# Kernel optimization log

Hardware: AMD Instinct MI355X
Metric: run time of the kernel (lower is better)

## Reference

```python
import jax, jax.numpy as jnp
import numpy as np

B, S, D, H = 4, 2048, 1024, 16
HD = D // H


def setup_inputs() -> dict:
    key = jax.random.key(0)
    ks = jax.random.split(key, 12)
    sc = 0.02
    inp = {
        "q": jax.random.normal(ks[0], (B, S, D), jnp.float32),
        "k": jax.random.normal(ks[1], (B, S, D), jnp.float32),
        "v": jax.random.normal(ks[2], (B, S, D), jnp.float32),
        "mask": jnp.tril(jnp.ones((S, S), jnp.int32))[None, None],  # causal [1,1,S,S]
        "Wq": jax.random.normal(ks[3], (D, D), jnp.float32) * sc,
        "bq": jnp.zeros((D,), jnp.float32),
        "Wk": jax.random.normal(ks[4], (D, D), jnp.float32) * sc,
        "bk": jnp.zeros((D,), jnp.float32),
        "Wv": jax.random.normal(ks[5], (D, D), jnp.float32) * sc,
        "bv": jnp.zeros((D,), jnp.float32),
        "Wo": jax.random.normal(ks[6], (D, D), jnp.float32) * sc,
        "bo": jnp.zeros((D,), jnp.float32),
    }
    return inp


def reference(q, k, v, mask, Wq, bq, Wk, bk, Wv, bv, Wo, bo):
    # Linear projections (torch Linear: x @ W.T + b)
    qh = (q @ Wq.T + bq).reshape(B, S, H, HD).transpose(0, 2, 1, 3)  # [B,H,S,hd]
    kh = (k @ Wk.T + bk).reshape(B, S, H, HD).transpose(0, 2, 1, 3)
    vh = (v @ Wv.T + bv).reshape(B, S, H, HD).transpose(0, 2, 1, 3)
    score = jnp.einsum("bhqd,bhkd->bhqk", qh, kh) / jnp.sqrt(jnp.float32(HD))
    score = jnp.where(mask == 0, jnp.float32(-10000.0), score)
    attn = jax.nn.softmax(score, axis=-1)
    out = jnp.einsum("bhqk,bhkd->bhqd", attn, vh)  # [B,H,S,hd]
    out = out.transpose(0, 2, 1, 3).reshape(B, S, D)
    return out @ Wo.T + bo
```

## Files before the change

### kernel.cpp

```cpp
#include <hip/hip_runtime.h>

#define S_LEN 2048
#define D_DIM 1024
#define NB    4
#define NH    16
#define HDIM  64
#define QSCL  0.18033688011112042f

typedef float  f32x4  __attribute__((ext_vector_type(4)));
typedef __bf16 bf16x4 __attribute__((ext_vector_type(4)));
typedef __bf16 bf16x8 __attribute__((ext_vector_type(8)));
typedef unsigned int u32x2 __attribute__((ext_vector_type(2)));
typedef unsigned int u32x4 __attribute__((ext_vector_type(4)));

static __device__ __forceinline__ f32x4 mfma16(bf16x8 a, bf16x8 b, f32x4 c) {
  return __builtin_amdgcn_mfma_f32_16x16x32_bf16(a, b, c, 0, 0, 0);
}
static __device__ __forceinline__ bf16x4 cvt4(f32x4 v) {
  return __builtin_convertvector(v, bf16x4);
}
static __device__ __forceinline__ bf16x8 cvt8(f32x4 lo, f32x4 hi) {
  bf16x4 a = cvt4(lo), b = cvt4(hi);
  bf16x8 r;
  r[0] = a[0]; r[1] = a[1]; r[2] = a[2]; r[3] = a[3];
  r[4] = b[0]; r[5] = b[1]; r[6] = b[2]; r[7] = b[3];
  return r;
}
static __device__ __forceinline__ void cp16(const void* g, void* l) {
  __builtin_amdgcn_global_load_lds(
      (const __attribute__((address_space(1))) unsigned int*)g,
      (__attribute__((address_space(3))) unsigned int*)l, 16, 0, 0);
}

__global__ __launch_bounds__(256) void conv_w(
    const float* __restrict__ Wq, const float* __restrict__ Wk,
    const float* __restrict__ Wv, const float* __restrict__ Wo,
    __bf16* __restrict__ out)
{
  const float* src;
  if (blockIdx.y == 0) src = Wq;
  else if (blockIdx.y == 1) src = Wk;
  else if (blockIdx.y == 2) src = Wv;
  else src = Wo;
  size_t i = ((size_t)blockIdx.x * 256 + threadIdx.x) * 4;
  f32x4 v = *(const f32x4*)(src + i);
  *(bf16x4*)(out + (size_t)blockIdx.y * (D_DIM * D_DIM) + i) = cvt4(v);
}

__global__ __launch_bounds__(256) void conv_a(
    const float* __restrict__ q, const float* __restrict__ k,
    const float* __restrict__ v, __bf16* __restrict__ out)
{
  const float* src;
  if (blockIdx.y == 0) src = q;
  else if (blockIdx.y == 1) src = k;
  else src = v;
  size_t i = ((size_t)blockIdx.x * 256 + threadIdx.x) * 4;
  f32x4 x = *(const f32x4*)(src + i);
  *(bf16x4*)(out + (size_t)blockIdx.y * ((size_t)NB * S_LEN * D_DIM) + i) = cvt4(x);
}

static __device__ __forceinline__ void proj_epilogue(
    f32x4 (&acc)[4][4], int z, int mbase, int nbase, int wm, int wn,
    int l15, int quad, const float* bias,
    __bf16* qh, __bf16* kh, __bf16* vt)
{
  const float scl = (z == 0) ? QSCL : 1.0f;
#pragma unroll
  for (int mt = 0; mt < 4; ++mt)
#pragma unroll
    for (int nt = 0; nt < 4; ++nt) {
      int n = nbase + wn + nt * 16 + l15;
      int h = n >> 6, hd = n & 63;
      float bb = bias[n];
      f32x4 vv = acc[mt][nt];
#pragma unroll
      for (int r = 0; r < 4; ++r) vv[r] = (vv[r] + bb) * scl;
      bf16x4 pv = cvt4(vv);
      int m0 = mbase + wm + mt * 16 + quad * 4;
      int b = m0 >> 11, s0 = m0 & 2047;
      if (z == 2) {
        *(bf16x4*)(vt + ((size_t)((b * NH + h) * HDIM + hd)) * S_LEN + s0) = pv;
      } else {
        __bf16* out = (z == 0) ? qh : kh;
#pragma unroll
        for (int r = 0; r < 4; ++r)
          out[((size_t)(b * NH + h) * S_LEN + s0 + r) * HDIM + hd] = pv[r];
      }
    }
}

__global__ __launch_bounds__(256, 4) void proj_bf16(
    const __bf16* __restrict__ abf, const __bf16* __restrict__ Wbf,
    const float* __restrict__ bq, const float* __restrict__ bk, const float* __restrict__ bv,
    __bf16* __restrict__ qh, __bf16* __restrict__ kh, __bf16* __restrict__ vt)
{
  const __bf16* A = abf + (size_t)blockIdx.z * ((size_t)NB * S_LEN * D_DIM);
  const __bf16* W = Wbf + (size_t)blockIdx.z * (D_DIM * D_DIM);
  const float* bias = (blockIdx.z == 0) ? bq : (blockIdx.z == 1) ? bk : bv;

  __shared__ __bf16 As[128 * 64];
  __shared__ __bf16 Bs[128 * 64];

  const int tid  = threadIdx.x;
  const int wave = tid >> 6;
  const int lane = tid & 63;
  const int l15  = lane & 15;
  const int quad = lane >> 4;
  const int mbase = blockIdx.x * 128;
  const int nbase = blockIdx.y * 128;
  const int wm = (wave & 1) * 64;
  const int wn = (wave >> 1) * 64;
  const int brow = lane >> 3;
  const int scol = ((lane & 7) ^ (brow & 7)) * 8;
  const int swz  = l15 & 7;

  f32x4 acc[4][4] = {};

  for (int kt = 0; kt < D_DIM; kt += 64) {
#pragma unroll
    for (int c = 0; c < 4; ++c) {
      int r = wave * 32 + c * 8 + brow;
      cp16(A + (size_t)(mbase + r) * D_DIM + kt + scol, As + r * 64);
      cp16(W + (size_t)(nbase + r) * D_DIM + kt + scol, Bs + r * 64);
    }
    __syncthreads();

#pragma unroll
    for (int k0 = 0; k0 < 2; ++k0) {
      bf16x8 af[4], bfr[4];
#pragma unroll
      for (int i = 0; i < 4; ++i) {
        int off = ((k0 * 4 + quad) ^ swz) * 8;
        af[i]  = *(const bf16x8*)(As + (wm + i * 16 + l15) * 64 + off);
        bfr[i] = *(const bf16x8*)(Bs + (wn + i * 16 + l15) * 64 + off);
      }
#pragma unroll
      for (int mt = 0; mt < 4; ++mt)
#pragma unroll
        for (int nt = 0; nt < 4; ++nt)
          acc[mt][nt] = mfma16(af[mt], bfr[nt], acc[mt][nt]);
    }
    __syncthreads();
  }

  proj_epilogue(acc, blockIdx.z, mbase, nbase, wm, wn, l15, quad, bias, qh, kh, vt);
}

__global__ __launch_bounds__(256, 2) void proj_f32(
    const float* __restrict__ qin, const float* __restrict__ kin, const float* __restrict__ vin,
    const __bf16* __restrict__ Wbf,
    const float* __restrict__ bq, const float* __restrict__ bk, const float* __restrict__ bv,
    __bf16* __restrict__ qh, __bf16* __restrict__ kh, __bf16* __restrict__ vt)
{
  const float* A; const float* bias;
  if (blockIdx.z == 0)      { A = qin; bias = bq; }
  else if (blockIdx.z == 1) { A = kin; bias = bk; }
  else                      { A = vin; bias = bv; }
  const __bf16* W = Wbf + (size_t)blockIdx.z * (D_DIM * D_DIM);

  __shared__ float  As[128 * 64];
  __shared__ __bf16 Bs[128 * 64];

  const int tid  = threadIdx.x;
  const int wave = tid >> 6;
  const int lane = tid & 63;
  const int l15  = lane & 15;
  const int quad = lane >> 4;
  const int mbase = blockIdx.x * 128;
  const int nbase = blockIdx.y * 128;
  const int wm = (wave & 1) * 64;
  const int wn = (wave >> 1) * 64;
  const int arow = lane >> 4;
  const int brow = lane >> 3;

  f32x4 acc[4][4] = {};

  for (int kt = 0; kt < D_DIM; kt += 64) {
#pragma unroll
    for (int c = 0; c < 8; ++c) {
      int rr = c * 4 + arow;
      int r  = wave * 32 + rr;
      int col = ((lane & 15) ^ (rr & 15)) * 4;
      cp16(A + (size_t)(mbase + r) * D_DIM + kt + col, As + r * 64);
    }
#pragma unroll
    for (int c = 0; c < 4; ++c) {
      int r  = wave * 32 + c * 8 + brow;
      int col = ((lane & 7) ^ (brow & 7)) * 8;
      cp16(W + (size_t)(nbase + r) * D_DIM + kt + col, Bs + r * 64);
    }
    __syncthreads();

#pragma unroll
    for (int k0 = 0; k0 < 2; ++k0) {
      bf16x8 af[4], bfr[4];
#pragma unroll
      for (int i = 0; i < 4; ++i) {
        const float* ap = As + (wm + i * 16 + l15) * 64;
        int c0 = k0 * 8 + quad * 2;
        f32x4 lo = *(const f32x4*)(ap + ((c0 ^ l15) * 4));
        f32x4 hi = *(const f32x4*)(ap + (((c0 + 1) ^ l15) * 4));
        af[i] = cvt8(lo, hi);
        bfr[i] = *(const bf16x8*)(Bs + (wn + i * 16 + l15) * 64 +
                                  (((k0 * 4 + quad) ^ (l15 & 7)) * 8));
      }
#pragma unroll
      for (int mt = 0; mt < 4; ++mt)
#pragma unroll
        for (int nt = 0; nt < 4; ++nt)
          acc[mt][nt] = mfma16(af[mt], bfr[nt], acc[mt][nt]);
    }
    __syncthreads();
  }

  proj_epilogue(acc, blockIdx.z, mbase, nbase, wm, wn, l15, quad, bias, qh, kh, vt);
}

__global__ __launch_bounds__(256, 4) void attn_kernel(
    const __bf16* __restrict__ qh, const __bf16* __restrict__ kh,
    const __bf16* __restrict__ vt, __bf16* __restrict__ ao)
{
  __shared__ __bf16 Kb[2][64 * 64];
  __shared__ __bf16 Vb[2][64 * 64];

  const int lin = blockIdx.x + (blockIdx.y << 4);
  const int xcd = lin & 7;
  const int idx = lin >> 3;
  const int u   = idx & 15;
  const int x   = (u & 1) ? (15 - (u >> 1)) : (u >> 1);
  const int bh  = xcd * 8 + (idx >> 4);

  const int qc0 = x, qc1 = 31 - x;
  const int last = qc1;

  const __bf16* qp = qh + (size_t)bh * S_LEN * HDIM;
  const __bf16* kp = kh + (size_t)bh * S_LEN * HDIM;
  const __bf16* vp = vt + (size_t)bh * HDIM * S_LEN;

  const int tid  = threadIdx.x;
  const int wave = tid >> 6;
  const int lane = tid & 63;
  const int l15  = lane & 15;
  const int quad = lane >> 4;
  const int w16  = wave * 16;
  const int srow = lane >> 3;
  const int scol = ((lane & 7) ^ srow) * 8;
  const int swz  = l15 & 7;
  const int b = bh >> 4, h = bh & 15;

  const int srcA = l15 + ((lane & 16) << 1);
  const int srcB = srcA + 16;
  const bool hiq = (lane & 32) != 0;

  bf16x8 fq[2][2];
#pragma unroll
  for (int j = 0; j < 2; ++j) {
    const int qb = (j ? qc1 : qc0) * 64;
    const __bf16* qrow = qp + (size_t)(qb + w16 + l15) * HDIM;
    fq[j][0] = *(const bf16x8*)(qrow + quad * 8);
    fq[j][1] = *(const bf16x8*)(qrow + 32 + quad * 8);
  }

  f32x4 accO[2][4] = {};
  float lp[2] = {0.f, 0.f};

#pragma unroll
  for (int c = 0; c < 2; ++c) {
    int rb = w16 + c * 8;
    cp16(kp + (size_t)(rb + srow) * HDIM + scol,  &Kb[0][rb * 64]);
    cp16(vp + (size_t)(rb + srow) * S_LEN + scol, &Vb[0][rb * 64]);
  }

  int cur = 0;
  for (int kt = 0; kt <= last; ++kt) {
    __syncthreads();

    if (kt < last) {
#pragma unroll
      for (int c = 0; c < 2; ++c) {
        int rb = w16 + c * 8;
        cp16(kp + (size_t)((kt + 1) * 64 + rb + srow) * HDIM + scol,
             &Kb[cur ^ 1][rb * 64]);
        cp16(vp + (size_t)(rb + srow) * S_LEN + (kt + 1) * 64 + scol,
             &Vb[cur ^ 1][rb * 64]);
      }
    }

    const __bf16* Kc = &Kb[cur][0];
    const __bf16* Vc = &Vb[cur][0];
    const bool act0 = (kt <= qc0);

    f32x4 sc[2][4] = {};
#pragma unroll
    for (int k0 = 0; k0 < 2; ++k0)
#pragma unroll
      for (int nt = 0; nt < 4; ++nt) {
        bf16x8 bk = *(const bf16x8*)(Kc + (nt * 16 + l15) * 64 +
                                     (((k0 * 4 + quad) ^ swz) * 8));
        if (act0) sc[0][nt] = mfma16(bk, fq[0][k0], sc[0][nt]);
        sc[1][nt] = mfma16(bk, fq[1][k0], sc[1][nt]);
      }

    bf16x8 pa[2][2];
#pragma unroll
    for (int j = 0; j < 2; ++j) {
      if (j == 0 && !act0) continue;
      const int qcj = j ? qc1 : qc0;
      unsigned int d0[4], d1[4];
      float lsn[4];
#pragma unroll
      for (int nt = 0; nt < 4; ++nt) {
        f32x4 p;
#pragma unroll
        for (int r = 0; r < 4; ++r) p[r] = __builtin_amdgcn_exp2f(sc[j][nt][r]);
        if (kt == qcj) {
#pragma unroll
          for (int r = 0; r < 4; ++r)
            if (nt * 16 + quad * 4 + r > w16 + l15) p[r] = 0.f;
        }
        lsn[nt] = (p[0] + p[1]) + (p[2] + p[3]);
        u32x2 w = __builtin_bit_cast(u32x2, cvt4(p));
        d0[nt] = w[0]; d1[nt] = w[1];
      }
      lp[j] += (lsn[0] + lsn[1]) + (lsn[2] + lsn[3]);

      u32x4 A0, A1;
#pragma unroll
      for (int dw = 0; dw < 4; ++dw) {
        const unsigned int* dd = (dw & 1) ? d1 : d0;
        const int src = (dw < 2) ? srcA : srcB;
        unsigned int t0 = (unsigned int)__shfl((int)dd[0], src);
        unsigned int t1 = (unsigned int)__shfl((int)dd[1], src);
        unsigned int t2 = (unsigned int)__shfl((int)dd[2], src);
        unsigned int t3 = (unsigned int)__shfl((int)dd[3], src);
        A0[dw] = hiq ? t1 : t0;
        A1[dw] = hiq ? t3 : t2;
      }
      pa[j][0] = __builtin_bit_cast(bf16x8, A0);
      pa[j][1] = __builtin_bit_cast(bf16x8, A1);
    }

#pragma unroll
    for (int k0 = 0; k0 < 2; ++k0)
#pragma unroll
      for (int nt = 0; nt < 4; ++nt) {
        bf16x8 bv = *(const bf16x8*)(Vc + (nt * 16 + l15) * 64 +
                                     (((k0 * 4 + quad) ^ swz) * 8));
        if (act0) accO[0][nt] = mfma16(pa[0][k0], bv, accO[0][nt]);
        accO[1][nt] = mfma16(pa[1][k0], bv, accO[1][nt]);
      }

    cur ^= 1;
  }

#pragma unroll
  for (int j = 0; j < 2; ++j) {
    float lf = lp[j];
    lf += __shfl_xor(lf, 16);
    lf += __shfl_xor(lf, 32);
    const int qb = (j ? qc1 : qc0) * 64;
#pragma unroll
    for (int r = 0; r < 4; ++r) {
      float inv = 1.0f / __shfl(lf, quad * 4 + r);
#pragma unroll
      for (int nt = 0; nt < 4; ++nt) accO[j][nt][r] *= inv;
    }
#pragma unroll
    for (int nt = 0; nt < 4; ++nt) {
      bf16x4 ob = cvt4(accO[j][nt]);
#pragma unroll
      for (int r = 0; r < 4; ++r) {
        int sr = qb + w16 + quad * 4 + r;
        ao[((size_t)b * S_LEN + sr) * D_DIM + h * HDIM + nt * 16 + l15] = ob[r];
      }
    }
  }
}

__global__ __launch_bounds__(256, 4) void out_gemm(
    const __bf16* __restrict__ Ain, const __bf16* __restrict__ Wbf,
    const float* __restrict__ bo, float* __restrict__ Cout)
{
  __shared__ __bf16 As[128 * 64];
  __shared__ __bf16 Bs[128 * 64];

  const int tid  = threadIdx.x;
  const int wave = tid >> 6;
  const int lane = tid & 63;
  const int l15  = lane & 15;
  const int quad = lane >> 4;
  const int mbase = blockIdx.x * 128;
  const int nbase = blockIdx.y * 128;
  const int wm = (wave & 1) * 64;
  const int wn = (wave >> 1) * 64;
  const int brow = lane >> 3;
  const int scol = ((lane & 7) ^ (brow & 7)) * 8;
  const int swz  = l15 & 7;

  f32x4 acc[4][4] = {};

  for (int kt = 0; kt < D_DIM; kt += 64) {
#pragma unroll
    for (int c = 0; c < 4; ++c) {
      int r = wave * 32 + c * 8 + brow;
      cp16(Ain + (size_t)(mbase + r) * D_DIM + kt + scol, As + r * 64);
      cp16(Wbf + (size_t)(nbase + r) * D_DIM + kt + scol, Bs + r * 64);
    }
    __syncthreads();

#pragma unroll
    for (int k0 = 0; k0 < 2; ++k0) {
      bf16x8 af[4], bfr[4];
#pragma unroll
      for (int i = 0; i < 4; ++i) {
        int off = ((k0 * 4 + quad) ^ swz) * 8;
        af[i]  = *(const bf16x8*)(As + (wm + i * 16 + l15) * 64 + off);
        bfr[i] = *(const bf16x8*)(Bs + (wn + i * 16 + l15) * 64 + off);
      }
#pragma unroll
      for (int mt = 0; mt < 4; ++mt)
#pragma unroll
        for (int nt = 0; nt < 4; ++nt)
          acc[mt][nt] = mfma16(af[mt], bfr[nt], acc[mt][nt]);
    }
    __syncthreads();
  }

#pragma unroll
  for (int mt = 0; mt < 4; ++mt)
#pragma unroll
    for (int nt = 0; nt < 4; ++nt) {
      int n = nbase + wn + nt * 16 + l15;
      float bb = bo[n];
      int m0 = mbase + wm + mt * 16 + quad * 4;
#pragma unroll
      for (int r = 0; r < 4; ++r)
        Cout[(size_t)(m0 + r) * D_DIM + n] = acc[mt][nt][r] + bb;
    }
}

extern "C" void kernel_launch(void* const* d_in, const int* in_sizes, int n_in,
                              void* d_out, int out_size, void* d_ws, size_t ws_size,
                              hipStream_t stream) {
  const float* q  = (const float*)d_in[0];
  const float* k  = (const float*)d_in[1];
  const float* v  = (const float*)d_in[2];
  const float* Wq = (const float*)d_in[4];
  const float* bq = (const float*)d_in[5];
  const float* Wk = (const float*)d_in[6];
  const float* bk = (const float*)d_in[7];
  const float* Wv = (const float*)d_in[8];
  const float* bv = (const float*)d_in[9];
  const float* Wo = (const float*)d_in[10];
  const float* bo = (const float*)d_in[11];

  __bf16* ws = (__bf16*)d_ws;
  const size_t WSZ = (size_t)D_DIM * D_DIM;
  const size_t NE  = (size_t)NB * S_LEN * D_DIM;
  __bf16* wbf = ws;
  __bf16* qh  = ws + 4 * WSZ;
  __bf16* kh  = qh + NE;
  __bf16* vt  = kh + NE;
  __bf16* ao  = vt + NE;
  __bf16* abf = vt + NE;
  const size_t NEED = (size_t)(4 * WSZ + 6 * NE) * sizeof(__bf16);

  const bool useBf16A = (ws_size >= NEED);

  conv_w<<<dim3(1024, 4), 256, 0, stream>>>(Wq, Wk, Wv, Wo, wbf);
  if (useBf16A) {
    conv_a<<<dim3(8192, 3), 256, 0, stream>>>(q, k, v, abf);
    proj_bf16<<<dim3(64, 8, 3), 256, 0, stream>>>(abf, wbf, bq, bk, bv, qh, kh, vt);
  } else {
    proj_f32<<<dim3(64, 8, 3), 256, 0, stream>>>(q, k, v, wbf, bq, bk, bv, qh, kh, vt);
  }
  attn_kernel<<<dim3(16, 64), 256, 0, stream>>>(qh, kh, vt, ao);
  out_gemm<<<dim3(64, 8), 256, 0, stream>>>(ao, wbf + 3 * WSZ, bo, (float*)d_out);
}
```

Baseline: 332.5 us.

## Permute K row mapping so softmax probabilities feed PV MFMA without shuffles

Reorders which key rows each lane reads for the QK^T MFMA so the resulting score layout matches the A-operand layout of the PV MFMA, and adjusts the LDS swizzle for K/V loads and V reads to match. This removes the per-tile cross-lane shuffles (16 __shfl per row block) and selects that repacked probabilities, replacing them with direct bf16 conversion. The causal mask index is recomputed for the permuted key order. The risk lies in the changed swizzle, which could introduce LDS bank conflicts or correctness errors if the permutation is inconsistent.

```diff
diff --git a/kernel.cpp b/kernel.cpp
--- a/kernel.cpp
+++ b/kernel.cpp
@@ -10,8 +10,6 @@
 typedef float  f32x4  __attribute__((ext_vector_type(4)));
 typedef __bf16 bf16x4 __attribute__((ext_vector_type(4)));
 typedef __bf16 bf16x8 __attribute__((ext_vector_type(8)));
-typedef unsigned int u32x2 __attribute__((ext_vector_type(2)));
-typedef unsigned int u32x4 __attribute__((ext_vector_type(4)));
 
 static __device__ __forceinline__ f32x4 mfma16(bf16x8 a, bf16x8 b, f32x4 c) {
   return __builtin_amdgcn_mfma_f32_16x16x32_bf16(a, b, c, 0, 0, 0);
@@ -245,13 +243,10 @@
   const int quad = lane >> 4;
   const int w16  = wave * 16;
   const int srow = lane >> 3;
-  const int scol = ((lane & 7) ^ srow) * 8;
   const int swz  = l15 & 7;
+  const int vswz = ((l15 >> 3) << 2) | (l15 & 3);
+  const int kr0  = ((l15 >> 2) << 3) | (l15 & 3);
   const int b = bh >> 4, h = bh & 15;
-
-  const int srcA = l15 + ((lane & 16) << 1);
-  const int srcB = srcA + 16;
-  const bool hiq = (lane & 32) != 0;
 
   bf16x8 fq[2][2];
 #pragma unroll
@@ -268,8 +263,9 @@
 #pragma unroll
   for (int c = 0; c < 2; ++c) {
     int rb = w16 + c * 8;
-    cp16(kp + (size_t)(rb + srow) * HDIM + scol,  &Kb[0][rb * 64]);
-    cp16(vp + (size_t)(rb + srow) * S_LEN + scol, &Vb[0][rb * 64]);
+    int sc2 = (((lane & 7) ^ (((c & 1) << 2) | (srow & 3)))) * 8;
+    cp16(kp + (size_t)(rb + srow) * HDIM + sc2, &Kb[0][rb * 64]);
+    cp16(vp + (size_t)(rb + srow) * S_LEN + sc2, &Vb[0][rb * 64]);
   }
 
   int cur = 0;
@@ -280,9 +276,10 @@
 #pragma unroll
       for (int c = 0; c < 2; ++c) {
         int rb = w16 + c * 8;
-        cp16(kp + (size_t)((kt + 1) * 64 + rb + srow) * HDIM + scol,
+        int sc2 = (((lane & 7) ^ (((c & 1) << 2) | (srow & 3)))) * 8;
+        cp16(kp + (size_t)((kt + 1) * 64 + rb + srow) * HDIM + sc2,
              &Kb[cur ^ 1][rb * 64]);
-        cp16(vp + (size_t)(rb + srow) * S_LEN + (kt + 1) * 64 + scol,
+        cp16(vp + (size_t)(rb + srow) * S_LEN + (kt + 1) * 64 + sc2,
              &Vb[cur ^ 1][rb * 64]);
       }
     }
@@ -296,7 +293,8 @@
     for (int k0 = 0; k0 < 2; ++k0)
 #pragma unroll
       for (int nt = 0; nt < 4; ++nt) {
-        bf16x8 bk = *(const bf16x8*)(Kc + (nt * 16 + l15) * 64 +
+        const int krow = kr0 + ((nt & 1) << 2) + ((nt >> 1) << 5);
+        bf16x8 bk = *(const bf16x8*)(Kc + krow * 64 +
                                      (((k0 * 4 + quad) ^ swz) * 8));
         if (act0) sc[0][nt] = mfma16(bk, fq[0][k0], sc[0][nt]);
         sc[1][nt] = mfma16(bk, fq[1][k0], sc[1][nt]);
@@ -307,38 +305,23 @@
     for (int j = 0; j < 2; ++j) {
       if (j == 0 && !act0) continue;
       const int qcj = j ? qc1 : qc0;
-      unsigned int d0[4], d1[4];
-      float lsn[4];
+      f32x4 pf[4];
 #pragma unroll
       for (int nt = 0; nt < 4; ++nt) {
-        f32x4 p;
-#pragma unroll
-        for (int r = 0; r < 4; ++r) p[r] = __builtin_amdgcn_exp2f(sc[j][nt][r]);
+#pragma unroll
+        for (int r = 0; r < 4; ++r) pf[nt][r] = __builtin_amdgcn_exp2f(sc[j][nt][r]);
         if (kt == qcj) {
 #pragma unroll
-          for (int r = 0; r < 4; ++r)
-            if (nt * 16 + quad * 4 + r > w16 + l15) p[r] = 0.f;
+          for (int r = 0; r < 4; ++r) {
+            int key = ((nt >> 1) << 5) + (quad << 3) + ((nt & 1) << 2) + r;
+            if (key > w16 + l15) pf[nt][r] = 0.f;
+          }
         }
-        lsn[nt] = (p[0] + p[1]) + (p[2] + p[3]);
-        u32x2 w = __builtin_bit_cast(u32x2, cvt4(p));
-        d0[nt] = w[0]; d1[nt] = w[1];
-      }
-      lp[j] += (lsn[0] + lsn[1]) + (lsn[2] + lsn[3]);
-
-      u32x4 A0, A1;
-#pragma unroll
-      for (int dw = 0; dw < 4; ++dw) {
-        const unsigned int* dd = (dw & 1) ? d1 : d0;
-        const int src = (dw < 2) ? srcA : srcB;
-        unsigned int t0 = (unsigned int)__shfl((int)dd[0], src);
-        unsigned int t1 = (unsigned int)__shfl((int)dd[1], src);
-        unsigned int t2 = (unsigned int)__shfl((int)dd[2], src);
-        unsigned int t3 = (unsigned int)__shfl((int)dd[3], src);
-        A0[dw] = hiq ? t1 : t0;
-        A1[dw] = hiq ? t3 : t2;
-      }
-      pa[j][0] = __builtin_bit_cast(bf16x8, A0);
-      pa[j][1] = __builtin_bit_cast(bf16x8, A1);
+      }
+      f32x4 lv = (pf[0] + pf[1]) + (pf[2] + pf[3]);
+      lp[j] += (lv[0] + lv[1]) + (lv[2] + lv[3]);
+      pa[j][0] = cvt8(pf[0], pf[1]);
+      pa[j][1] = cvt8(pf[2], pf[3]);
     }
 
 #pragma unroll
@@ -346,7 +329,7 @@
 #pragma unroll
       for (int nt = 0; nt < 4; ++nt) {
         bf16x8 bv = *(const bf16x8*)(Vc + (nt * 16 + l15) * 64 +
-                                     (((k0 * 4 + quad) ^ swz) * 8));
+                                     (((k0 * 4 + quad) ^ vswz) * 8));
         if (act0) accO[0][nt] = mfma16(pa[0][k0], bv, accO[0][nt]);
         accO[1][nt] = mfma16(pa[1][k0], bv, accO[1][nt]);
       }
```

New measurement: 306.1 us. -7.9%, faster.
